# Kernel tuning notes

Hardware: AMD Instinct MI355X
Metric: run time of the kernel (lower is better)

The kernel has to match this reference:

```python
import jax, jax.numpy as jnp
import numpy as np
from jax import lax

D_MODEL = 256; D_HEAD = 32; NHEAD = 8; WIN = 8; TOPK = 8; DMID = 1024
B = 2; H = 128; WD = 128
BN_EPS = 1e-5; ATT_EPS = 1e-6

def _bn(x, g, b, m, v):
    # inference-mode BatchNorm2d over NCHW
    s = g / jnp.sqrt(v + BN_EPS)
    return x * s[None, :, None, None] + (b - m * s)[None, :, None, None]

def _gelu(x):
    return jax.nn.gelu(x, approximate=False)  # torch nn.GELU default (erf)

def _conv1x1(x, w, bias=None):
    y = jnp.einsum('bchw,oc->bohw', x, w)
    if bias is not None:
        y = y + bias[None, :, None, None]
    return y

def _to_win(t):
    b, d, h, wd = t.shape
    nh, nw = h // WIN, wd // WIN
    t = t.reshape(b, d, nh, WIN, nw, WIN).transpose(0, 2, 4, 3, 5, 1)
    return t.reshape(b, nh * nw, WIN * WIN, d)

def _from_win(m, h, wd):
    b, n, w2, d = m.shape
    nh, nw = h // WIN, wd // WIN
    m = m.reshape(b, nh, nw, WIN, WIN, d).transpose(0, 5, 1, 3, 2, 4)
    return m.reshape(b, d, h, wd)

def _linear_attention(q, k, v):
    # LoFTR linear attention. q: [n, L, H, D]; k, v: [n, S, H, D]
    Q = jax.nn.elu(q) + 1.0
    K = jax.nn.elu(k) + 1.0
    s_len = v.shape[1]
    vals = v / s_len
    KV = jnp.einsum('nshd,nshv->nhdv', K, vals)
    Z = 1.0 / (jnp.einsum('nlhd,nhd->nlh', Q, K.sum(axis=1)) + ATT_EPS)
    return jnp.einsum('nlhd,nhdv,nlh->nlhv', Q, KV, Z) * s_len

def _topk_window_attention(q, k, v):
    # partition into WINxWIN windows, select top-K key windows per query window
    # by mean-pooled window similarity, gather them, attend within each window.
    b, d, h, wd = q.shape
    qw, kw, vw = _to_win(q), _to_win(k), _to_win(v)  # [b, N, W2, d]
    n = qw.shape[1]; w2 = WIN * WIN
    sim = jnp.einsum('bnd,bmd->bnm', qw.mean(axis=2), kw.mean(axis=2))
    idx = lax.top_k(sim, TOPK)[1]  # [b, N, K]
    gather = jax.vmap(lambda t, i: t[i])  # over batch: [N,W2,d],[N,K] -> [N,K,W2,d]
    kg = gather(kw, idx).reshape(b, n, TOPK * w2, d)
    vg = gather(vw, idx).reshape(b, n, TOPK * w2, d)
    Q = qw.reshape(b * n, w2, NHEAD, D_HEAD)
    K = kg.reshape(b * n, TOPK * w2, NHEAD, D_HEAD)
    V = vg.reshape(b * n, TOPK * w2, NHEAD, D_HEAD)
    out = _linear_attention(Q, K, V).reshape(b, n, w2, d)
    return _from_win(out, h, wd)

def _forward(x0, bn0_g, bn0_b, bn0_m, bn0_v, q_w, k_w, v_w, merge_w, merge_b,
             mlp_w1, bn1_g, bn1_b, bn1_m, bn1_v, mlp_dw,
             bn2_g, bn2_b, bn2_m, bn2_v, mlp_w2, bn3_g, bn3_b, bn3_m, bn3_v):
    _x = _gelu(_bn(x0, bn0_g, bn0_b, bn0_m, bn0_v))  # pre_normact (x1 = x0)
    q = _conv1x1(_x, q_w); k = _conv1x1(_x, k_w); v = _conv1x1(_x, v_w)
    msg = _topk_window_attention(q, k, v)
    x = x0 + _conv1x1(msg, merge_w, merge_b)  # merge + residual (DropPath=id)
    # MB mlp block: 1x1 -> BN -> GELU -> dw3x3 -> BN -> GELU -> 1x1 -> BN
    y = _conv1x1(x, mlp_w1)
    y = _gelu(_bn(y, bn1_g, bn1_b, bn1_m, bn1_v))
    y = lax.conv_general_dilated(y, mlp_dw, (1, 1), 'SAME',
                                 feature_group_count=DMID,
                                 dimension_numbers=('NCHW', 'OIHW', 'NCHW'))
    y = _gelu(_bn(y, bn2_g, bn2_b, bn2_m, bn2_v))
    y = _conv1x1(y, mlp_w2)
    y = _bn(y, bn3_g, bn3_b, bn3_m, bn3_v)
    return x + y

def setup_inputs() -> dict:
    ks = jax.random.split(jax.random.key(0), 26)
    nrm = lambda i, shape, s=1.0: jax.random.normal(ks[i], shape, jnp.float32) * s
    uni = lambda i, shape: jax.random.uniform(ks[i], shape, jnp.float32, 0.5, 1.5)
    sc = float(1.0 / np.sqrt(D_MODEL))
    return {
        'x0': nrm(0, (B, D_MODEL, H, WD)),
        'bn0_g': uni(1, (D_MODEL,)), 'bn0_b': nrm(2, (D_MODEL,), 0.1),
        'bn0_m': nrm(3, (D_MODEL,), 0.1), 'bn0_v': uni(4, (D_MODEL,)),
        'q_w': nrm(5, (D_MODEL, D_MODEL), sc),
        'k_w': nrm(6, (D_MODEL, D_MODEL), sc),
        'v_w': nrm(7, (D_MODEL, D_MODEL), sc),
        'merge_w': nrm(8, (D_MODEL, D_MODEL), sc), 'merge_b': nrm(9, (D_MODEL,), 0.1),
        'mlp_w1': nrm(10, (DMID, D_MODEL), sc),
        'bn1_g': uni(11, (DMID,)), 'bn1_b': nrm(12, (DMID,), 0.1),
        'bn1_m': nrm(13, (DMID,), 0.1), 'bn1_v': uni(14, (DMID,)),
        'mlp_dw': nrm(15, (DMID, 1, 3, 3), 1.0 / 3.0),
        'bn2_g': uni(16, (DMID,)), 'bn2_b': nrm(17, (DMID,), 0.1),
        'bn2_m': nrm(18, (DMID,), 0.1), 'bn2_v': uni(19, (DMID,)),
        'mlp_w2': nrm(20, (D_MODEL, DMID), float(1.0 / np.sqrt(DMID))),
        'bn3_g': uni(21, (D_MODEL,)), 'bn3_b': nrm(22, (D_MODEL,), 0.1),
        'bn3_m': nrm(23, (D_MODEL,), 0.1), 'bn3_v': uni(24, (D_MODEL,)),
    }

def reference(x0, bn0_g, bn0_b, bn0_m, bn0_v, q_w, k_w, v_w, merge_w, merge_b,
              mlp_w1, bn1_g, bn1_b, bn1_m, bn1_v, mlp_dw,
              bn2_g, bn2_b, bn2_m, bn2_v, mlp_w2, bn3_g, bn3_b, bn3_m, bn3_v):
    return _forward(x0, bn0_g, bn0_b, bn0_m, bn0_v, q_w, k_w, v_w, merge_w, merge_b,
                    mlp_w1, bn1_g, bn1_b, bn1_m, bn1_v, mlp_dw,
                    bn2_g, bn2_b, bn2_m, bn2_v, mlp_w2, bn3_g, bn3_b, bn3_m, bn3_v)
```

## Files before the change

kernel.cpp:

```cpp
#include <hip/hip_runtime.h>
#include <hip/hip_bf16.h>
#include <type_traits>

typedef __hip_bfloat16 bf16;
typedef __attribute__((ext_vector_type(8))) short s16x8;
typedef __attribute__((ext_vector_type(4))) short s16x4;
typedef __attribute__((ext_vector_type(4))) float f32x4;

#define DEVI __device__ __forceinline__

DEVI float bf2f(bf16 x) { return __bfloat162float(x); }
DEVI float to_f(float x) { return x; }
DEVI float to_f(bf16 x) { return __bfloat162float(x); }
DEVI float gelu_f(float x) {
  const float y = x * 0.7071067811865476f;
  const float a = fabsf(y);
  const float t = __builtin_amdgcn_rcpf(1.0f + 0.3275911f * a);
  const float p = t * (0.254829592f + t * (-0.284496736f +
                  t * (1.421413741f + t * (-1.453152027f + t * 1.061405429f))));
  const float e = __expf(-a * a);
  const float erfv = copysignf(1.0f - p * e, y);
  return 0.5f * x * (1.0f + erfv);
}
DEVI float elu1(float x) { return x > 0.f ? x + 1.f : __expf(x); }
DEVI float s2f(short s) {
  unsigned u = ((unsigned)(unsigned short)s) << 16;
  float f; __builtin_memcpy(&f, &u, 4); return f;
}
DEVI short f2s(float x) {
  bf16 h = __float2bfloat16(x);
  short s; __builtin_memcpy(&s, &h, 2); return s;
}

__global__ void detect_kernel(const void* x0, int* dflag) {
  const int t = threadIdx.x;
  const bf16* p = (const bf16*)x0;
  float v = bf2f(p[t * 2]);
  bool ok = (fabsf(v) <= 64.0f);
  unsigned long long m = __ballot(ok);
  if (t == 0) dflag[0] = (m == ~0ull) ? 0 : 1;
}

template <typename TIN>
__global__ __launch_bounds__(256) void bnprep_kernel(
    const int* dflag, int want,
    const TIN* g0, const TIN* b0, const TIN* m0, const TIN* v0,
    const TIN* g1, const TIN* b1, const TIN* m1, const TIN* v1,
    const TIN* g2, const TIN* b2, const TIN* m2, const TIN* v2,
    const TIN* g3, const TIN* b3, const TIN* m3, const TIN* v3,
    const TIN* mb, float* out)
{
  if (dflag[0] != want) return;
  int t = threadIdx.x;
  {
    float s = to_f(g0[t]) / sqrtf(to_f(v0[t]) + 1e-5f);
    out[t] = s; out[256 + t] = to_f(b0[t]) - to_f(m0[t]) * s;
  }
  for (int i = t; i < 1024; i += 256) {
    float s = to_f(g1[i]) / sqrtf(to_f(v1[i]) + 1e-5f);
    out[512 + i] = s; out[1536 + i] = to_f(b1[i]) - to_f(m1[i]) * s;
  }
  for (int i = t; i < 1024; i += 256) {
    float s = to_f(g2[i]) / sqrtf(to_f(v2[i]) + 1e-5f);
    out[2560 + i] = s; out[3584 + i] = to_f(b2[i]) - to_f(m2[i]) * s;
  }
  {
    float s = to_f(g3[t]) / sqrtf(to_f(v3[t]) + 1e-5f);
    out[4608 + t] = s; out[4864 + t] = to_f(b3[t]) - to_f(m3[t]) * s;
    out[5120 + t] = to_f(mb[t]);
  }
}

template <typename TIN>
__global__ __launch_bounds__(256) void wconv_kernel(
    const int* dflag, int want,
    const TIN* qw, const TIN* kw, const TIN* vw, const TIN* mw,
    const TIN* w1, const TIN* w2, const TIN* dw, bf16* dst)
{
  if (dflag[0] != want) return;
  int i = blockIdx.x * 256 + threadIdx.x;
  if (i >= 795648) return;
  const TIN* src; int off;
  if (i < 262144) {
    src = (i < 65536) ? qw : (i < 131072) ? kw : (i < 196608) ? vw : mw;
    off = i & 65535;
  } else if (i < 524288) { src = w1; off = i - 262144; }
  else if (i < 786432) { src = w2; off = i - 524288; }
  else {
    src = dw;
    const int o = i - 786432;
    const int tap = o >> 10, m = o & 1023;
    off = m * 9 + tap;
    if (o >= 9216) return;
  }
  dst[i] = __float2bfloat16(to_f(src[off]));
}

template <typename TIN>
__global__ __launch_bounds__(256) void prenorm_t_kernel(
    const int* dflag, int want, const TIN* __restrict__ x0,
    const float* __restrict__ bn, bf16* __restrict__ xhat_t)
{
  if (dflag[0] != want) return;
  __shared__ float T[128][67];
  const int t = threadIdx.x;
  const int tile = blockIdx.x;
  const int b = tile >> 8;
  const int p0 = (tile & 255) * 64;
  const long xbase = (long)b * 4194304 + p0;
  const int px_off = (t & 7) * 8;
  const int chr = t >> 3;
  const int ch8 = (t & 15) * 8;
  const int pxw = t >> 4;
  #pragma unroll
  for (int pass = 0; pass < 2; ++pass) {
    const int Hc = pass * 128;
    __syncthreads();
    #pragma unroll
    for (int cc = 0; cc < 4; ++cc) {
      const int ch = Hc + chr + 32 * cc;
      const TIN* xp = x0 + (long)ch * 16384 + xbase + px_off;
      float v[8];
      if constexpr (sizeof(TIN) == 2) {
        const s16x8 r = *(const s16x8*)xp;
        #pragma unroll
        for (int j = 0; j < 8; ++j) v[j] = s2f(r[j]);
      } else {
        const float4 a = *(const float4*)xp;
        const float4 c = *(const float4*)(xp + 4);
        v[0] = a.x; v[1] = a.y; v[2] = a.z; v[3] = a.w;
        v[4] = c.x; v[5] = c.y; v[6] = c.z; v[7] = c.w;
      }
      const float s0 = bn[ch], t0 = bn[256 + ch];
      #pragma unroll
      for (int j = 0; j < 8; ++j) v[j] = gelu_f(v[j] * s0 + t0);
      float* Tr = &T[chr + 32 * cc][px_off];
      #pragma unroll
      for (int j = 0; j < 8; ++j) Tr[j] = v[j];
    }
    __syncthreads();
    #pragma unroll
    for (int it = 0; it < 4; ++it) {
      const int px = pxw + 16 * it;
      alignas(16) short o[8];
      #pragma unroll
      for (int j = 0; j < 8; ++j) o[j] = f2s(T[ch8 + j][px]);
      *(uint4*)(xhat_t + (long)(b * 16384 + p0 + px) * 256 + Hc + ch8) =
          *(const uint4*)o;
    }
  }
}

template <int MODE, typename TRES = bf16>
__global__ __launch_bounds__(256) void mfma_gemm(
    const int* dflag, int want,
    const bf16* __restrict__ in, const bf16* __restrict__ w,
    void* __restrict__ out, long obase, const void* __restrict__ resv,
    const float* __restrict__ sv, const float* __restrict__ tv,
    float* __restrict__ aux, int N, int M, int K)
{
  if (want >= 0 && dflag[0] != want) return;
  alignas(16) __shared__ char smem[(MODE <= 2) ? 20480 : 34816];
  bf16* inT = (bf16*)smem;
  bf16* wT  = (bf16*)(smem + 10240);
  const int t = threadIdx.x;
  const int n0 = blockIdx.x * 128, m0 = blockIdx.y * 128;
  const int sr = t >> 1, sk = (t & 1) * 16;
  const int wid = t >> 6, lane = t & 63;
  const int nw = (wid & 1) * 64, mw = (wid >> 1) * 64;
  const int l15 = lane & 15, quad = lane >> 4;
  f32x4 acc[4][4];
  #pragma unroll
  for (int i = 0; i < 4; ++i)
    #pragma unroll
    for (int j = 0; j < 4; ++j) acc[i][j] = 0.f;
  long inRow;
  if (MODE == 4) {
    const int bb4 = n0 >> 14, w0 = (n0 & 16383) >> 6;
    const int win = w0 + (sr >> 6);
    const int rr = (sr >> 3) & 7, cc = sr & 7;
    inRow = ((long)(bb4 * 16384 + ((win >> 4) * 8 + rr) * 128
                    + (win & 15) * 8 + cc)) * K + sk;
  } else {
    inRow = (long)(n0 + sr) * K + sk;
  }
  const long wRow = (long)(m0 + sr) * K + sk;
  uint4 a0 = *(const uint4*)(in + inRow);
  uint4 a1 = *(const uint4*)(in + inRow + 8);
  uint4 b0 = *(const uint4*)(w + wRow);
  uint4 b1 = *(const uint4*)(w + wRow + 8);
  for (int k0 = 0; k0 < K; k0 += 32) {
    __syncthreads();
    *(uint4*)(inT + sr * 40 + sk) = a0;
    *(uint4*)(inT + sr * 40 + sk + 8) = a1;
    *(uint4*)(wT + sr * 40 + sk) = b0;
    *(uint4*)(wT + sr * 40 + sk + 8) = b1;
    __syncthreads();
    if (k0 + 32 < K) {
      a0 = *(const uint4*)(in + inRow + k0 + 32);
      a1 = *(const uint4*)(in + inRow + k0 + 40);
      b0 = *(const uint4*)(w + wRow + k0 + 32);
      b1 = *(const uint4*)(w + wRow + k0 + 40);
    }
    s16x8 af[4], bfv[4];
    #pragma unroll
    for (int i = 0; i < 4; ++i)
      af[i] = *(const s16x8*)(inT + (nw + i * 16 + l15) * 40 + quad * 8);
    #pragma unroll
    for (int i = 0; i < 4; ++i)
      bfv[i] = *(const s16x8*)(wT + (mw + i * 16 + l15) * 40 + quad * 8);
    #pragma unroll
    for (int i = 0; i < 4; ++i)
      #pragma unroll
      for (int j = 0; j < 4; ++j)
        acc[i][j] = __builtin_amdgcn_mfma_f32_16x16x32_bf16(af[i], bfv[j], acc[i][j], 0, 0, 0);
  }
  if (MODE <= 2) {
    bf16* ob = (bf16*)out;
    const bool doelu = (MODE == 0) && (m0 < 512);
    #pragma unroll
    for (int i = 0; i < 4; ++i) {
      #pragma unroll
      for (int r = 0; r < 4; ++r) {
        const int n = n0 + nw + i * 16 + quad * 4 + r;
        #pragma unroll
        for (int j = 0; j < 4; ++j) {
          const int m = m0 + mw + j * 16 + l15;
          float vv = acc[i][j][r];
          if (MODE == 0) { if (doelu) vv = elu1(vv); }
          if (MODE == 1) {
            const TRES* res = (const TRES*)resv;
            vv += sv[m] + to_f(res[(long)(n >> 14) * 4194304
                                   + (long)m * 16384 + (n & 16383)]);
          }
          if (MODE == 2) vv = gelu_f(vv * sv[m] + tv[m]);
          ob[(long)n * M + m] = __float2bfloat16(vv);
        }
      }
    }
  } else {
    const int isf = (MODE == 3) ? dflag[0] : 0;
    __syncthreads();
    bf16* T = (bf16*)smem;
    #pragma unroll
    for (int i = 0; i < 4; ++i)
      #pragma unroll
      for (int r = 0; r < 4; ++r) {
        const int n = nw + i * 16 + quad * 4 + r;
        #pragma unroll
        for (int j = 0; j < 4; ++j) {
          const int m = mw + j * 16 + l15;
          float vv = acc[i][j][r];
          if (MODE == 3)
            vv = vv * sv[m0 + m] + tv[m0 + m]
               + bf2f(((const bf16*)resv)[(long)(n0 + n) * 256 + m0 + m]);
          else { if (m0 + m < 256) vv = elu1(vv); }
          T[m * 136 + n] = __float2bfloat16(vv);
        }
      }
    __syncthreads();
    const int mr = t >> 1, half = (t & 1) * 64;
    if (MODE == 4) {
      const int bb4 = n0 >> 14, w0 = (n0 & 16383) >> 6;
      const int gm = m0 + mr;
      bf16* bo = (bf16*)out;
      #pragma unroll
      for (int jj = 0; jj < 8; ++jj) {
        const int C = half + jj * 8;
        const int win = w0 + (C >> 6);
        const int pxc = (C & 63) >> 3;
        *(uint4*)(bo + ((long)(bb4 * 256 + win) << 15) + pxc * 4096 + gm * 8) =
            *(const uint4*)(T + mr * 136 + C);
      }
      if (m0 < 256) {
        float s = 0.f;
        const bf16* Tr = T + mr * 136 + half;
        #pragma unroll
        for (int c8 = 0; c8 < 8; ++c8) {
          const s16x8 v = *(const s16x8*)(Tr + c8 * 8);
          #pragma unroll
          for (int e = 0; e < 8; ++e) s += s2f(v[e]);
        }
        aux[(long)(bb4 * 256 + w0 + (half >> 6)) * 256 + gm] = s;
      }
    } else {
      const int bb3 = n0 >> 14, nloc = n0 & 16383;
      if (!isf) {
        bf16* bo = (bf16*)out + obase + (long)bb3 * 4194304;
        #pragma unroll
        for (int jj = 0; jj < 8; ++jj)
          *(uint4*)(bo + (long)(m0 + mr) * 16384 + nloc + half + jj * 8) =
              *(const uint4*)(T + mr * 136 + half + jj * 8);
      } else {
        float* fo = (float*)out + obase + (long)bb3 * 4194304;
        #pragma unroll
        for (int jj = 0; jj < 8; ++jj)
          #pragma unroll
          for (int e = 0; e < 8; ++e)
            fo[(long)(m0 + mr) * 16384 + nloc + half + jj * 8 + e] =
                bf2f(T[mr * 136 + half + jj * 8 + e]);
      }
    }
  }
}

template <typename TIN>
__global__ __launch_bounds__(256) void xmean_kernel(const int* dflag, int want,
                                                    const TIN* __restrict__ x0,
                                                    const float* __restrict__ bn,
                                                    float* __restrict__ xm)
{
  if (dflag[0] != want) return;
  int tid = blockIdx.x * 256 + threadIdx.x;
  int n = tid & 255, c = (tid >> 8) & 255, b = tid >> 16;
  const float s0 = bn[c], t0 = bn[256 + c];
  const long base = (long)b * 4194304 + (long)c * 16384 + ((n >> 4) * 8) * 128 + (n & 15) * 8;
  float s = 0.f;
  #pragma unroll
  for (int r = 0; r < 8; ++r)
    #pragma unroll
    for (int cc = 0; cc < 8; ++cc)
      s += gelu_f(to_f(x0[base + r * 128 + cc]) * s0 + t0);
  xm[tid] = s * 0.015625f;
}

template <typename TIN>
__global__ __launch_bounds__(256) void meanproj_kernel(const int* dflag, int want,
    const TIN* __restrict__ qw, const TIN* __restrict__ kw,
    const float* __restrict__ xm, float* __restrict__ qm, float* __restrict__ km)
{
  if (dflag[0] != want) return;
  int tid = blockIdx.x * 256 + threadIdx.x;
  int nw = tid & 255, o = (tid >> 8) & 255, b = tid >> 16;
  float sq = 0.f, sk = 0.f;
  for (int c = 0; c < 256; ++c) {
    const float x = xm[(b * 256 + c) * 256 + nw];
    sq += to_f(qw[o * 256 + c]) * x;
    sk += to_f(kw[o * 256 + c]) * x;
  }
  qm[(b * 256 + o) * 256 + nw] = sq;
  km[(b * 256 + o) * 256 + nw] = sk;
}

__global__ __launch_bounds__(256) void topk_kernel(const float* __restrict__ qm,
                                                   const float* __restrict__ km,
                                                   int* __restrict__ topki)
{
  const int nq = blockIdx.x, b = blockIdx.y, t = threadIdx.x;
  float sim = 0.f;
  for (int c = 0; c < 256; ++c)
    sim += qm[(b * 256 + c) * 256 + nq] * km[(b * 256 + c) * 256 + t];
  __shared__ float vals[256];
  __shared__ float rv[256];
  __shared__ int ri[256];
  vals[t] = sim;
  __syncthreads();
  for (int j = 0; j < 8; ++j) {
    rv[t] = vals[t]; ri[t] = t;
    __syncthreads();
    for (int off = 128; off > 0; off >>= 1) {
      if (t < off) {
        float v2 = rv[t + off]; int i2 = ri[t + off];
        if (v2 > rv[t] || (v2 == rv[t] && i2 < ri[t])) { rv[t] = v2; ri[t] = i2; }
      }
      __syncthreads();
    }
    const int w = ri[0];
    if (t == 0) topki[(b * 256 + nq) * 8 + j] = w;
    __syncthreads();
    if (t == w) vals[t] = -3.0e38f;
    __syncthreads();
  }
}

__global__ __launch_bounds__(256) void attn_kernel(
    const bf16* __restrict__ qbuf, const bf16* __restrict__ kvT,
    const int* __restrict__ topki, const float* __restrict__ S,
    bf16* __restrict__ msg)
{
  __shared__ bf16 kvB[10240];
  __shared__ float ksum_s[256];
  __shared__ float zs2[512];
  const int n = blockIdx.x, b = blockIdx.y, t = threadIdx.x;
  const long bpix = (long)b * 16384;
  const int lane = t & 63, wid = t >> 6;
  const int l15 = lane & 15, quad = lane >> 4;
  const int h0 = wid * 2;
  f32x4 kvacc[2][2][2];
  #pragma unroll
  for (int a = 0; a < 2; ++a)
    #pragma unroll
    for (int c = 0; c < 2; ++c)
      #pragma unroll
      for (int d = 0; d < 2; ++d) kvacc[a][c][d] = 0.f;
  int wsel[8];
  #pragma unroll
  for (int j = 0; j < 8; ++j) wsel[j] = topki[(b * 256 + n) * 8 + j];

  const long kvTb = (long)b * 8388608;
  #pragma unroll 8
  for (int ck = 0; ck < 16; ++ck) {
    const bf16* base = kvT + kvTb + ((long)wsel[ck >> 1] << 15)
                     + ((ck & 1) * 4 + quad) * 4096;
    #pragma unroll
    for (int hs = 0; hs < 2; ++hs) {
      const int cb = (h0 + hs) * 32;
      const s16x8 a0 = *(const s16x8*)(base + (cb + l15) * 8);
      const s16x8 a1 = *(const s16x8*)(base + (cb + 16 + l15) * 8);
      const s16x8 b0 = *(const s16x8*)(base + (256 + cb + l15) * 8);
      const s16x8 b1 = *(const s16x8*)(base + (256 + cb + 16 + l15) * 8);
      kvacc[hs][0][0] = __builtin_amdgcn_mfma_f32_16x16x32_bf16(a0, b0, kvacc[hs][0][0], 0, 0, 0);
      kvacc[hs][0][1] = __builtin_amdgcn_mfma_f32_16x16x32_bf16(a0, b1, kvacc[hs][0][1], 0, 0, 0);
      kvacc[hs][1][0] = __builtin_amdgcn_mfma_f32_16x16x32_bf16(a1, b0, kvacc[hs][1][0], 0, 0, 0);
      kvacc[hs][1][1] = __builtin_amdgcn_mfma_f32_16x16x32_bf16(a1, b1, kvacc[hs][1][1], 0, 0, 0);
    }
  }

  {
    float ks = 0.f;
    #pragma unroll
    for (int j = 0; j < 8; ++j)
      ks += S[((long)b * 256 + wsel[j]) * 256 + t];
    ksum_s[t] = ks;
  }
  #pragma unroll
  for (int hs = 0; hs < 2; ++hs)
    #pragma unroll
    for (int vt = 0; vt < 2; ++vt) {
      const int row = (h0 + hs) * 32 + vt * 16 + l15;
      #pragma unroll
      for (int dt = 0; dt < 2; ++dt) {
        const f32x4 kv = kvacc[hs][dt][vt];
        uint2 u;
        u.x = (unsigned)(unsigned short)f2s(kv[0])
            | ((unsigned)(unsigned short)f2s(kv[1]) << 16);
        u.y = (unsigned)(unsigned short)f2s(kv[2])
            | ((unsigned)(unsigned short)f2s(kv[3]) << 16);
        *(uint2*)(kvB + row * 40 + dt * 16 + quad * 4) = u;
      }
    }
  __syncthreads();

  const int qh0 = (n >> 4) * 8, qw0 = (n & 15) * 8;
  #pragma unroll
  for (int rep = 0; rep < 2; ++rep) {
    const int idx = t + rep * 256;
    const int l = idx >> 3, hh = idx & 7;
    const long gp = bpix + (qh0 + (l >> 3)) * 128 + qw0 + (l & 7);
    const bf16* qp = qbuf + gp * 256 + hh * 32;
    float dot = 0.f;
    #pragma unroll
    for (int k4 = 0; k4 < 4; ++k4) {
      const s16x8 q8 = *(const s16x8*)(qp + k4 * 8);
      const float4 kA = *(const float4*)(ksum_s + hh * 32 + k4 * 8);
      const float4 kB = *(const float4*)(ksum_s + hh * 32 + k4 * 8 + 4);
      dot += s2f(q8[0]) * kA.x + s2f(q8[1]) * kA.y
           + s2f(q8[2]) * kA.z + s2f(q8[3]) * kA.w
           + s2f(q8[4]) * kB.x + s2f(q8[5]) * kB.y
           + s2f(q8[6]) * kB.z + s2f(q8[7]) * kB.w;
    }
    zs2[hh * 64 + l] = 1.f / (dot + 1e-6f);
  }
  __syncthreads();

  #pragma unroll
  for (int hs = 0; hs < 2; ++hs) {
    const int h = h0 + hs;
    const s16x8 B0 = *(const s16x8*)(kvB + (h * 32 + l15) * 40 + quad * 8);
    const s16x8 B1 = *(const s16x8*)(kvB + (h * 32 + 16 + l15) * 40 + quad * 8);
    #pragma unroll
    for (int i = 0; i < 4; ++i) {
      const int lq = i * 16 + l15;
      const long gpa = bpix + (qh0 + (lq >> 3)) * 128 + qw0 + (lq & 7);
      const s16x8 A = *(const s16x8*)(qbuf + gpa * 256 + h * 32 + quad * 8);
      f32x4 o0 = 0.f, o1 = 0.f;
      o0 = __builtin_amdgcn_mfma_f32_16x16x32_bf16(A, B0, o0, 0, 0, 0);
      o1 = __builtin_amdgcn_mfma_f32_16x16x32_bf16(A, B1, o1, 0, 0, 0);
      const float4 z4 = *(const float4*)(zs2 + h * 64 + i * 16 + quad * 4);
      const float zr[4] = {z4.x, z4.y, z4.z, z4.w};
      #pragma unroll
      for (int r = 0; r < 4; ++r) {
        const int lo = i * 16 + quad * 4 + r;
        const long opix = bpix + (qh0 + (lo >> 3)) * 128 + qw0 + (lo & 7);
        msg[opix * 256 + h * 32 + l15] = __float2bfloat16(o0[r] * zr[r]);
        msg[opix * 256 + h * 32 + 16 + l15] = __float2bfloat16(o1[r] * zr[r]);
      }
    }
  }
}

__global__ __launch_bounds__(256) void dwconv_kernel(const bf16* __restrict__ y1,
                                                     const bf16* __restrict__ wdw,
                                                     const float* __restrict__ s2,
                                                     const float* __restrict__ t2,
                                                     bf16* __restrict__ y2)
{
  const int strip = blockIdx.x;
  const int bb = strip >> 11;
  const int sl = strip & 2047;
  const int x0 = (sl & 15) * 8;
  const int yy = sl >> 4;
  const int m0 = threadIdx.x * 4;
  const bf16* y1b = y1 + (long)bb * 16777216;
  bf16* y2b = y2 + (long)bb * 16777216;
  float wv[9][4];
  #pragma unroll
  for (int tap = 0; tap < 9; ++tap) {
    const s16x4 w4 = *(const s16x4*)(wdw + tap * 1024 + m0);
    #pragma unroll
    for (int e = 0; e < 4; ++e) wv[tap][e] = s2f(w4[e]);
  }
  float acc[8][4];
  #pragma unroll
  for (int p = 0; p < 8; ++p)
    #pragma unroll
    for (int e = 0; e < 4; ++e) acc[p][e] = 0.f;
  #pragma unroll
  for (int ky = 0; ky < 3; ++ky) {
    const int row = yy + ky - 1;
    if ((unsigned)row < 128u) {
      const bf16* rp = y1b + (long)row * 131072 + m0;
      #pragma unroll
      for (int cr = 0; cr < 10; ++cr) {
        const int xc = x0 + cr - 1;
        if ((unsigned)xc < 128u) {
          const s16x4 v4 = *(const s16x4*)(rp + (long)xc * 1024);
          float vf[4];
          #pragma unroll
          for (int e = 0; e < 4; ++e) vf[e] = s2f(v4[e]);
          #pragma unroll
          for (int kx = 0; kx < 3; ++kx) {
            const int p = cr - kx;
            if (p >= 0 && p < 8) {
              #pragma unroll
              for (int e = 0; e < 4; ++e)
                acc[p][e] += wv[ky * 3 + kx][e] * vf[e];
            }
          }
        }
      }
    }
  }
  const float4 sv = *(const float4*)(s2 + m0);
  const float4 tv = *(const float4*)(t2 + m0);
  #pragma unroll
  for (int p = 0; p < 8; ++p) {
    s16x4 o;
    o[0] = f2s(gelu_f(acc[p][0] * sv.x + tv.x));
    o[1] = f2s(gelu_f(acc[p][1] * sv.y + tv.y));
    o[2] = f2s(gelu_f(acc[p][2] * sv.z + tv.z));
    o[3] = f2s(gelu_f(acc[p][3] * sv.w + tv.w));
    *(s16x4*)(y2b + (long)(yy * 128 + x0 + p) * 1024 + m0) = o;
  }
}

template <typename TIN>
static void stage_dtype_pre(int want, void* const* d_in, hipStream_t stream,
                            const int* dflag, bf16* wb, float* bnbuf,
                            bf16* xhat_t, float* xmean, float* qm, float* km)
{
  bnprep_kernel<TIN><<<1, 256, 0, stream>>>(dflag, want,
      (const TIN*)d_in[1],  (const TIN*)d_in[2],  (const TIN*)d_in[3],  (const TIN*)d_in[4],
      (const TIN*)d_in[11], (const TIN*)d_in[12], (const TIN*)d_in[13], (const TIN*)d_in[14],
      (const TIN*)d_in[16], (const TIN*)d_in[17], (const TIN*)d_in[18], (const TIN*)d_in[19],
      (const TIN*)d_in[21], (const TIN*)d_in[22], (const TIN*)d_in[23], (const TIN*)d_in[24],
      (const TIN*)d_in[9], bnbuf);
  wconv_kernel<TIN><<<3108, 256, 0, stream>>>(dflag, want,
      (const TIN*)d_in[5], (const TIN*)d_in[6], (const TIN*)d_in[7], (const TIN*)d_in[8],
      (const TIN*)d_in[10], (const TIN*)d_in[20], (const TIN*)d_in[15], wb);
  prenorm_t_kernel<TIN><<<512, 256, 0, stream>>>(dflag, want,
      (const TIN*)d_in[0], bnbuf, xhat_t);
  xmean_kernel<TIN><<<512, 256, 0, stream>>>(dflag, want, (const TIN*)d_in[0], bnbuf, xmean);
  meanproj_kernel<TIN><<<512, 256, 0, stream>>>(dflag, want,
      (const TIN*)d_in[5], (const TIN*)d_in[6], xmean, qm, km);
}

extern "C" void kernel_launch(void* const* d_in, const int* in_sizes, int n_in,
                              void* d_out, int out_size, void* d_ws, size_t ws_size,
                              hipStream_t stream) {
  (void)n_in; (void)out_size;
  char* W = (char*)d_ws;
  bf16*  xhat_t = (bf16*)(W);
  bf16*  xres   = (bf16*)(W);
  float* Swin   = (float*)(W + 16777216);
  bf16*  qbuf   = (bf16*)(W + 33554432);
  bf16*  kvT    = (bf16*)(W + 50331648);
  bf16*  msg    = (bf16*)(W + 83886080);
  char*  S      = W + 100663296;
  bf16*  wb     = (bf16*)(S);
  bf16*  wmb    = wb + 196608;
  bf16*  w1b    = wb + 262144;
  bf16*  w2b    = wb + 524288;
  bf16*  wdwb   = wb + 786432;
  float* bnbuf  = (float*)(S + 1591296);
  float* xmean  = (float*)(S + 1612800);
  float* qm     = (float*)(S + 2137088);
  float* km     = (float*)(S + 2661376);
  int*   topki  = (int*)(S + 3185664);
  int*   dflag  = (int*)(S + 3202048);
  const bool big = (ws_size == 0) || (ws_size >= 171966464ull);
  bf16*  y1     = (bf16*)(W + 33554432);
  bf16*  y2     = big ? (bf16*)(W + 104857600) : (bf16*)(W + 67108864);

  int known = -1;
  if (in_sizes) {
    if (in_sizes[0] == 16777216) known = 0;
    else if (in_sizes[0] == 33554432) known = 1;
  }

  detect_kernel<<<1, 64, 0, stream>>>(d_in[0], dflag);

  if (known != 1)
    stage_dtype_pre<bf16>(0, d_in, stream, dflag, wb, bnbuf, xhat_t, xmean, qm, km);
  if (known != 0)
    stage_dtype_pre<float>(1, d_in, stream, dflag, wb, bnbuf, xhat_t, xmean, qm, km);

  mfma_gemm<0><<<dim3(256, 2), 256, 0, stream>>>(dflag, -1,
      xhat_t, wb, (void*)qbuf, 0, nullptr, nullptr, nullptr, nullptr, 32768, 256, 256);
  mfma_gemm<4><<<dim3(256, 4), 256, 0, stream>>>(dflag, -1,
      xhat_t, wb + 65536, (void*)kvT, 0, nullptr, nullptr, nullptr, Swin, 32768, 512, 256);

  topk_kernel<<<dim3(256, 2), 256, 0, stream>>>(qm, km, topki);
  attn_kernel<<<dim3(256, 2), 256, 0, stream>>>(qbuf, kvT, topki, Swin, msg);

  if (known != 1)
    mfma_gemm<1, bf16><<<dim3(256, 2), 256, 0, stream>>>(dflag, 0,
        msg, wmb, (void*)xres, 0, d_in[0], bnbuf + 5120, nullptr, nullptr, 32768, 256, 256);
  if (known != 0)
    mfma_gemm<1, float><<<dim3(256, 2), 256, 0, stream>>>(dflag, 1,
        msg, wmb, (void*)xres, 0, d_in[0], bnbuf + 5120, nullptr, nullptr, 32768, 256, 256);

  if (big) {
    mfma_gemm<2><<<dim3(256, 8), 256, 0, stream>>>(dflag, -1,
        xres, w1b, (void*)y1, 0, nullptr, bnbuf + 512, bnbuf + 1536, nullptr, 32768, 1024, 256);
    dwconv_kernel<<<4096, 256, 0, stream>>>(y1, wdwb, bnbuf + 2560, bnbuf + 3584, y2);
    mfma_gemm<3><<<dim3(256, 2), 256, 0, stream>>>(dflag, -1,
        y2, w2b, d_out, 0, xres, bnbuf + 4608, bnbuf + 4864, nullptr, 32768, 256, 1024);
  } else {
    for (int b = 0; b < 2; ++b) {
      bf16* xres_b = xres + (long)b * 4194304;
      mfma_gemm<2><<<dim3(128, 8), 256, 0, stream>>>(dflag, -1,
          xres_b, w1b, (void*)y1, 0, nullptr, bnbuf + 512, bnbuf + 1536, nullptr, 16384, 1024, 256);
      dwconv_kernel<<<2048, 256, 0, stream>>>(y1, wdwb, bnbuf + 2560, bnbuf + 3584, y2);
      mfma_gemm<3><<<dim3(128, 2), 256, 0, stream>>>(dflag, -1,
          y2, w2b, d_out, (long)b * 4194304, xres_b,
          bnbuf + 4608, bnbuf + 4864, nullptr, 16384, 256, 1024);
    }
  }
}
```

Measured before the change: 404.0 us.

## Fuse window-mean into prenorm, shuffle-based topk, staged residual epilogue, skip dtype detect

Window-mean partial sums are now computed inside the prenorm transpose kernel and reduced by a small kernel, so x0 is no longer re-read and GELU is no longer recomputed in a separate xmean pass. The topk selection now uses wavefront shuffles instead of a shared-memory tree reduction. The merge-GEMM residual is staged through shared memory for coalesced reads of the NCHW input. When the input size identifies the dtype, the detect kernel and the device flag checks are skipped. The meanproj loop is also split across four accumulators. The cost is an extra scratch buffer and one more small launch.

New measurement: 389.2 us (median of 3 runs). 3.6% less time.

```diff
diff --git a/kernel.cpp b/kernel.cpp
--- a/kernel.cpp
+++ b/kernel.cpp
@@ -50,7 +50,7 @@
     const TIN* g3, const TIN* b3, const TIN* m3, const TIN* v3,
     const TIN* mb, float* out)
 {
-  if (dflag[0] != want) return;
+  if (want >= 0 && dflag[0] != want) return;
   int t = threadIdx.x;
   {
     float s = to_f(g0[t]) / sqrtf(to_f(v0[t]) + 1e-5f);
@@ -77,7 +77,7 @@
     const TIN* qw, const TIN* kw, const TIN* vw, const TIN* mw,
     const TIN* w1, const TIN* w2, const TIN* dw, bf16* dst)
 {
-  if (dflag[0] != want) return;
+  if (want >= 0 && dflag[0] != want) return;
   int i = blockIdx.x * 256 + threadIdx.x;
   if (i >= 795648) return;
   const TIN* src; int off;
@@ -99,14 +99,19 @@
 template <typename TIN>
 __global__ __launch_bounds__(256) void prenorm_t_kernel(
     const int* dflag, int want, const TIN* __restrict__ x0,
-    const float* __restrict__ bn, bf16* __restrict__ xhat_t)
-{
-  if (dflag[0] != want) return;
+    const float* __restrict__ bn, bf16* __restrict__ xhat_t,
+    float* __restrict__ xmp)
+{
+  if (want >= 0 && dflag[0] != want) return;
   __shared__ float T[128][67];
   const int t = threadIdx.x;
   const int tile = blockIdx.x;
   const int b = tile >> 8;
-  const int p0 = (tile & 255) * 64;
+  const int rc = tile & 255;
+  const int p0 = rc * 64;
+  const int row = rc >> 1, colh = rc & 1;
+  const int win = (row >> 3) * 16 + colh * 8 + (t & 7);
+  const int wrow = row & 7;
   const long xbase = (long)b * 4194304 + p0;
   const int px_off = (t & 7) * 8;
   const int chr = t >> 3;
@@ -134,6 +139,10 @@
       const float s0 = bn[ch], t0 = bn[256 + ch];
       #pragma unroll
       for (int j = 0; j < 8; ++j) v[j] = gelu_f(v[j] * s0 + t0);
+      float s8 = v[0];
+      #pragma unroll
+      for (int j = 1; j < 8; ++j) s8 += v[j];
+      xmp[(((b * 8 + wrow) * 256 + ch) << 8) + win] = s8;
       float* Tr = &T[chr + 32 * cc][px_off];
       #pragma unroll
       for (int j = 0; j < 8; ++j) Tr[j] = v[j];
@@ -151,16 +160,28 @@
   }
 }
 
+__global__ __launch_bounds__(256) void xred_kernel(const float* __restrict__ xmp,
+                                                   float* __restrict__ xm)
+{
+  const int tid = blockIdx.x * 256 + threadIdx.x;
+  const int nw = tid & 255, c = (tid >> 8) & 255, b = tid >> 16;
+  float s = 0.f;
+  #pragma unroll
+  for (int w = 0; w < 8; ++w)
+    s += xmp[(((b * 8 + w) * 256 + c) << 8) + nw];
+  xm[tid] = s * 0.015625f;
+}
+
 template <int MODE, typename TRES = bf16>
 __global__ __launch_bounds__(256) void mfma_gemm(
-    const int* dflag, int want,
+    const int* dflag, int want, int isfp,
     const bf16* __restrict__ in, const bf16* __restrict__ w,
     void* __restrict__ out, long obase, const void* __restrict__ resv,
     const float* __restrict__ sv, const float* __restrict__ tv,
     float* __restrict__ aux, int N, int M, int K)
 {
   if (want >= 0 && dflag[0] != want) return;
-  alignas(16) __shared__ char smem[(MODE <= 2) ? 20480 : 34816];
+  alignas(16) __shared__ char smem[(MODE == 0 || MODE == 2) ? 20480 : 34816];
   bf16* inT = (bf16*)smem;
   bf16* wT  = (bf16*)(smem + 10240);
   const int t = threadIdx.x;
@@ -215,7 +236,7 @@
       for (int j = 0; j < 4; ++j)
         acc[i][j] = __builtin_amdgcn_mfma_f32_16x16x32_bf16(af[i], bfv[j], acc[i][j], 0, 0, 0);
   }
-  if (MODE <= 2) {
+  if (MODE == 0 || MODE == 2) {
     bf16* ob = (bf16*)out;
     const bool doelu = (MODE == 0) && (m0 < 512);
     #pragma unroll
@@ -228,18 +249,55 @@
           const int m = m0 + mw + j * 16 + l15;
           float vv = acc[i][j][r];
           if (MODE == 0) { if (doelu) vv = elu1(vv); }
-          if (MODE == 1) {
-            const TRES* res = (const TRES*)resv;
-            vv += sv[m] + to_f(res[(long)(n >> 14) * 4194304
-                                   + (long)m * 16384 + (n & 16383)]);
-          }
           if (MODE == 2) vv = gelu_f(vv * sv[m] + tv[m]);
           ob[(long)n * M + m] = __float2bfloat16(vv);
         }
       }
     }
+  } else if (MODE == 1) {
+    __syncthreads();
+    bf16* xL = (bf16*)smem;
+    {
+      const int bb = n0 >> 14, nloc = n0 & 16383;
+      const int chl = t >> 1, pxh = (t & 1) * 64;
+      const TRES* xp = (const TRES*)resv + (long)bb * 4194304
+                     + (long)(m0 + chl) * 16384 + nloc + pxh;
+      alignas(16) short tmp[64];
+      if constexpr (std::is_same<TRES, float>::value) {
+        #pragma unroll
+        for (int q = 0; q < 16; ++q) {
+          const float4 f = *(const float4*)(xp + q * 4);
+          tmp[q * 4 + 0] = f2s(f.x); tmp[q * 4 + 1] = f2s(f.y);
+          tmp[q * 4 + 2] = f2s(f.z); tmp[q * 4 + 3] = f2s(f.w);
+        }
+      } else {
+        #pragma unroll
+        for (int q = 0; q < 8; ++q)
+          *(s16x8*)(tmp + q * 8) = *(const s16x8*)((const bf16*)xp + q * 8);
+      }
+      bf16* xd = xL + chl * 132 + pxh;
+      #pragma unroll
+      for (int q = 0; q < 8; ++q)
+        *(uint4*)(xd + q * 8) = *(const uint4*)(tmp + q * 8);
+    }
+    __syncthreads();
+    bf16* ob = (bf16*)out;
+    #pragma unroll
+    for (int i = 0; i < 4; ++i)
+      #pragma unroll
+      for (int r = 0; r < 4; ++r) {
+        const int nl = nw + i * 16 + quad * 4 + r;
+        const int n = n0 + nl;
+        #pragma unroll
+        for (int j = 0; j < 4; ++j) {
+          const int ml = mw + j * 16 + l15;
+          const int m = m0 + ml;
+          const float vv = acc[i][j][r] + sv[m] + bf2f(xL[ml * 132 + nl]);
+          ob[(long)n * 256 + m] = __float2bfloat16(vv);
+        }
+      }
   } else {
-    const int isf = (MODE == 3) ? dflag[0] : 0;
+    const int isf = (MODE == 3) ? (isfp >= 0 ? isfp : dflag[0]) : 0;
     __syncthreads();
     bf16* T = (bf16*)smem;
     #pragma unroll
@@ -305,41 +363,27 @@
 }
 
 template <typename TIN>
-__global__ __launch_bounds__(256) void xmean_kernel(const int* dflag, int want,
-                                                    const TIN* __restrict__ x0,
-                                                    const float* __restrict__ bn,
-                                                    float* __restrict__ xm)
-{
-  if (dflag[0] != want) return;
-  int tid = blockIdx.x * 256 + threadIdx.x;
-  int n = tid & 255, c = (tid >> 8) & 255, b = tid >> 16;
-  const float s0 = bn[c], t0 = bn[256 + c];
-  const long base = (long)b * 4194304 + (long)c * 16384 + ((n >> 4) * 8) * 128 + (n & 15) * 8;
-  float s = 0.f;
-  #pragma unroll
-  for (int r = 0; r < 8; ++r)
-    #pragma unroll
-    for (int cc = 0; cc < 8; ++cc)
-      s += gelu_f(to_f(x0[base + r * 128 + cc]) * s0 + t0);
-  xm[tid] = s * 0.015625f;
-}
-
-template <typename TIN>
 __global__ __launch_bounds__(256) void meanproj_kernel(const int* dflag, int want,
     const TIN* __restrict__ qw, const TIN* __restrict__ kw,
     const float* __restrict__ xm, float* __restrict__ qm, float* __restrict__ km)
 {
-  if (dflag[0] != want) return;
+  if (want >= 0 && dflag[0] != want) return;
   int tid = blockIdx.x * 256 + threadIdx.x;
   int nw = tid & 255, o = (tid >> 8) & 255, b = tid >> 16;
-  float sq = 0.f, sk = 0.f;
-  for (int c = 0; c < 256; ++c) {
-    const float x = xm[(b * 256 + c) * 256 + nw];
-    sq += to_f(qw[o * 256 + c]) * x;
-    sk += to_f(kw[o * 256 + c]) * x;
-  }
-  qm[(b * 256 + o) * 256 + nw] = sq;
-  km[(b * 256 + o) * 256 + nw] = sk;
+  float q0 = 0.f, q1 = 0.f, q2 = 0.f, q3 = 0.f;
+  float k0 = 0.f, k1 = 0.f, k2 = 0.f, k3 = 0.f;
+  for (int c = 0; c < 256; c += 4) {
+    const float x0v = xm[((b * 256 + c) << 8) + nw];
+    const float x1v = xm[((b * 256 + c + 1) << 8) + nw];
+    const float x2v = xm[((b * 256 + c + 2) << 8) + nw];
+    const float x3v = xm[((b * 256 + c + 3) << 8) + nw];
+    q0 += to_f(qw[o * 256 + c]) * x0v;     k0 += to_f(kw[o * 256 + c]) * x0v;
+    q1 += to_f(qw[o * 256 + c + 1]) * x1v; k1 += to_f(kw[o * 256 + c + 1]) * x1v;
+    q2 += to_f(qw[o * 256 + c + 2]) * x2v; k2 += to_f(kw[o * 256 + c + 2]) * x2v;
+    q3 += to_f(qw[o * 256 + c + 3]) * x3v; k3 += to_f(kw[o * 256 + c + 3]) * x3v;
+  }
+  qm[((b * 256 + o) << 8) + nw] = (q0 + q1) + (q2 + q3);
+  km[((b * 256 + o) << 8) + nw] = (k0 + k1) + (k2 + k3);
 }
 
 __global__ __launch_bounds__(256) void topk_kernel(const float* __restrict__ qm,
@@ -347,28 +391,31 @@
                                                    int* __restrict__ topki)
 {
   const int nq = blockIdx.x, b = blockIdx.y, t = threadIdx.x;
+  const int lane = t & 63, wid = t >> 6;
   float sim = 0.f;
   for (int c = 0; c < 256; ++c)
-    sim += qm[(b * 256 + c) * 256 + nq] * km[(b * 256 + c) * 256 + t];
+    sim += qm[((b * 256 + c) << 8) + nq] * km[((b * 256 + c) << 8) + t];
   __shared__ float vals[256];
-  __shared__ float rv[256];
-  __shared__ int ri[256];
+  __shared__ float rv4[4];
+  __shared__ int ri4[4];
   vals[t] = sim;
   __syncthreads();
   for (int j = 0; j < 8; ++j) {
-    rv[t] = vals[t]; ri[t] = t;
-    __syncthreads();
-    for (int off = 128; off > 0; off >>= 1) {
-      if (t < off) {
-        float v2 = rv[t + off]; int i2 = ri[t + off];
-        if (v2 > rv[t] || (v2 == rv[t] && i2 < ri[t])) { rv[t] = v2; ri[t] = i2; }
-      }
-      __syncthreads();
-    }
-    const int w = ri[0];
-    if (t == 0) topki[(b * 256 + nq) * 8 + j] = w;
-    __syncthreads();
-    if (t == w) vals[t] = -3.0e38f;
+    float v = vals[t]; int idx = t;
+    #pragma unroll
+    for (int off = 1; off < 64; off <<= 1) {
+      const float v2 = __shfl_xor(v, off);
+      const int i2 = __shfl_xor(idx, off);
+      if (v2 > v || (v2 == v && i2 < idx)) { v = v2; idx = i2; }
+    }
+    if (lane == 0) { rv4[wid] = v; ri4[wid] = idx; }
+    __syncthreads();
+    float bv = rv4[0]; int bi = ri4[0];
+    #pragma unroll
+    for (int w2 = 1; w2 < 4; ++w2)
+      if (rv4[w2] > bv || (rv4[w2] == bv && ri4[w2] < bi)) { bv = rv4[w2]; bi = ri4[w2]; }
+    if (t == 0) topki[(b * 256 + nq) * 8 + j] = bi;
+    if (t == bi) vals[t] = -3.0e38f;
     __syncthreads();
   }
 }
@@ -557,7 +604,7 @@
 template <typename TIN>
 static void stage_dtype_pre(int want, void* const* d_in, hipStream_t stream,
                             const int* dflag, bf16* wb, float* bnbuf,
-                            bf16* xhat_t, float* xmean, float* qm, float* km)
+                            bf16* xhat_t, float* xmp)
 {
   bnprep_kernel<TIN><<<1, 256, 0, stream>>>(dflag, want,
       (const TIN*)d_in[1],  (const TIN*)d_in[2],  (const TIN*)d_in[3],  (const TIN*)d_in[4],
@@ -569,10 +616,7 @@
       (const TIN*)d_in[5], (const TIN*)d_in[6], (const TIN*)d_in[7], (const TIN*)d_in[8],
       (const TIN*)d_in[10], (const TIN*)d_in[20], (const TIN*)d_in[15], wb);
   prenorm_t_kernel<TIN><<<512, 256, 0, stream>>>(dflag, want,
-      (const TIN*)d_in[0], bnbuf, xhat_t);
-  xmean_kernel<TIN><<<512, 256, 0, stream>>>(dflag, want, (const TIN*)d_in[0], bnbuf, xmean);
-  meanproj_kernel<TIN><<<512, 256, 0, stream>>>(dflag, want,
-      (const TIN*)d_in[5], (const TIN*)d_in[6], xmean, qm, km);
+      (const TIN*)d_in[0], bnbuf, xhat_t, xmp);
 }
 
 extern "C" void kernel_launch(void* const* d_in, const int* in_sizes, int n_in,
@@ -583,6 +627,7 @@
   bf16*  xhat_t = (bf16*)(W);
   bf16*  xres   = (bf16*)(W);
   float* Swin   = (float*)(W + 16777216);
+  float* xmp    = (float*)(W + 17301504);
   bf16*  qbuf   = (bf16*)(W + 33554432);
   bf16*  kvT    = (bf16*)(W + 50331648);
   bf16*  msg    = (bf16*)(W + 83886080);
@@ -593,7 +638,7 @@
   bf16*  w2b    = wb + 524288;
   bf16*  wdwb   = wb + 786432;
   float* bnbuf  = (float*)(S + 1591296);
-  float* xmean  = (float*)(S + 1612800);
+  float* xm     = (float*)(S + 1612800);
   float* qm     = (float*)(S + 2137088);
   float* km     = (float*)(S + 2661376);
   int*   topki  = (int*)(S + 3185664);
@@ -608,41 +653,49 @@
     else if (in_sizes[0] == 33554432) known = 1;
   }
 
-  detect_kernel<<<1, 64, 0, stream>>>(d_in[0], dflag);
+  if (known < 0) detect_kernel<<<1, 64, 0, stream>>>(d_in[0], dflag);
 
   if (known != 1)
-    stage_dtype_pre<bf16>(0, d_in, stream, dflag, wb, bnbuf, xhat_t, xmean, qm, km);
+    stage_dtype_pre<bf16>(known == 0 ? -1 : 0, d_in, stream, dflag, wb, bnbuf, xhat_t, xmp);
   if (known != 0)
-    stage_dtype_pre<float>(1, d_in, stream, dflag, wb, bnbuf, xhat_t, xmean, qm, km);
-
-  mfma_gemm<0><<<dim3(256, 2), 256, 0, stream>>>(dflag, -1,
+    stage_dtype_pre<float>(known == 1 ? -1 : 1, d_in, stream, dflag, wb, bnbuf, xhat_t, xmp);
+
+  xred_kernel<<<512, 256, 0, stream>>>(xmp, xm);
+  if (known != 1)
+    meanproj_kernel<bf16><<<512, 256, 0, stream>>>(dflag, known == 0 ? -1 : 0,
+        (const bf16*)d_in[5], (const bf16*)d_in[6], xm, qm, km);
+  if (known != 0)
+    meanproj_kernel<float><<<512, 256, 0, stream>>>(dflag, known == 1 ? -1 : 1,
+        (const float*)d_in[5], (const float*)d_in[6], xm, qm, km);
+
+  mfma_gemm<0><<<dim3(256, 2), 256, 0, stream>>>(dflag, -1, -1,
       xhat_t, wb, (void*)qbuf, 0, nullptr, nullptr, nullptr, nullptr, 32768, 256, 256);
-  mfma_gemm<4><<<dim3(256, 4), 256, 0, stream>>>(dflag, -1,
+  mfma_gemm<4><<<dim3(256, 4), 256, 0, stream>>>(dflag, -1, -1,
       xhat_t, wb + 65536, (void*)kvT, 0, nullptr, nullptr, nullptr, Swin, 32768, 512, 256);
 
   topk_kernel<<<dim3(256, 2), 256, 0, stream>>>(qm, km, topki);
   attn_kernel<<<dim3(256, 2), 256, 0, stream>>>(qbuf, kvT, topki, Swin, msg);
 
   if (known != 1)
-    mfma_gemm<1, bf16><<<dim3(256, 2), 256, 0, stream>>>(dflag, 0,
+    mfma_gemm<1, bf16><<<dim3(256, 2), 256, 0, stream>>>(dflag, known == 0 ? -1 : 0, -1,
         msg, wmb, (void*)xres, 0, d_in[0], bnbuf + 5120, nullptr, nullptr, 32768, 256, 256);
   if (known != 0)
-    mfma_gemm<1, float><<<dim3(256, 2), 256, 0, stream>>>(dflag, 1,
+    mfma_gemm<1, float><<<dim3(256, 2), 256, 0, stream>>>(dflag, known == 1 ? -1 : 1, -1,
         msg, wmb, (void*)xres, 0, d_in[0], bnbuf + 5120, nullptr, nullptr, 32768, 256, 256);
 
   if (big) {
-    mfma_gemm<2><<<dim3(256, 8), 256, 0, stream>>>(dflag, -1,
+    mfma_gemm<2><<<dim3(256, 8), 256, 0, stream>>>(dflag, -1, -1,
         xres, w1b, (void*)y1, 0, nullptr, bnbuf + 512, bnbuf + 1536, nullptr, 32768, 1024, 256);
     dwconv_kernel<<<4096, 256, 0, stream>>>(y1, wdwb, bnbuf + 2560, bnbuf + 3584, y2);
-    mfma_gemm<3><<<dim3(256, 2), 256, 0, stream>>>(dflag, -1,
+    mfma_gemm<3><<<dim3(256, 2), 256, 0, stream>>>(dflag, -1, known,
         y2, w2b, d_out, 0, xres, bnbuf + 4608, bnbuf + 4864, nullptr, 32768, 256, 1024);
   } else {
     for (int b = 0; b < 2; ++b) {
       bf16* xres_b = xres + (long)b * 4194304;
-      mfma_gemm<2><<<dim3(128, 8), 256, 0, stream>>>(dflag, -1,
+      mfma_gemm<2><<<dim3(128, 8), 256, 0, stream>>>(dflag, -1, -1,
           xres_b, w1b, (void*)y1, 0, nullptr, bnbuf + 512, bnbuf + 1536, nullptr, 16384, 1024, 256);
       dwconv_kernel<<<2048, 256, 0, stream>>>(y1, wdwb, bnbuf + 2560, bnbuf + 3584, y2);
-      mfma_gemm<3><<<dim3(128, 2), 256, 0, stream>>>(dflag, -1,
+      mfma_gemm<3><<<dim3(128, 2), 256, 0, stream>>>(dflag, -1, known,
           y2, w2b, d_out, (long)b * 4194304, xres_b,
           bnbuf + 4608, bnbuf + 4864, nullptr, 16384, 256, 1024);
     }
```
